# Performance work log

Measured on AMD Instinct MI355X. Metric: run time of the kernel, lower is better.

## Reference

```python
import jax, jax.numpy as jnp
import numpy as np

B, L, K1, P = 16, 224, 8192, 16  # batch, spectral bands, pixels, endmembers
LEAKY_SLOPE = 0.01  # torch nn.LeakyReLU default


def setup_inputs() -> dict:
    key = jax.random.key(0)
    ks = jax.random.split(key, 7)
    return {
        "a": jax.random.normal(ks[0], (B, P, K1), jnp.float32),
        "d2": jax.random.normal(ks[1], (B, P, K1), jnp.float32),
        "y": jax.random.normal(ks[2], (B, L, K1), jnp.float32),
        "w3_w": jax.random.normal(ks[3], (P, P), jnp.float32) * 0.1,  # Conv1d(P,P,1) weight squeezed
        "b3_w": jax.random.normal(ks[4], (P, P), jnp.float32) * 0.1,
        "w3_c": jax.random.normal(ks[5], (1, L, P), jnp.float32),     # kernel codebook
        "sigma": jnp.ones((1,), jnp.float32) * 2.0,
        "ca_w": jax.random.normal(ks[6], (2, P), jnp.float32) * 0.1,  # CA Conv1d(P,2,1) weight squeezed
    }


def reference(a, d2, y, w3_w, b3_w, w3_c, sigma, ca_w):
    # h2 = Conv1d(P,P,1)(a - d2)  -> pointwise matmul over channel dim
    h2 = jnp.einsum('pq,bqn->bpn', w3_w, a - d2)  # (B,P,K1)

    # GaussianKernelLayer: pairwise L2 distances between y pixels (B,L,K1)
    # and codebook columns w3_c (1,L,P), via the GEMM identity
    # ||u-v||^2 = ||u||^2 + ||v||^2 - 2 u.v  (avoids the (B,L,K1,P) broadcast).
    y_sq = jnp.sum(y * y, axis=1)            # (B,K1)
    c_sq = jnp.sum(w3_c * w3_c, axis=1)      # (1,P)
    cross = jnp.einsum('blk,olp->bkp', y, w3_c)  # (B,K1,P)
    dist_sq = jnp.maximum(y_sq[:, :, None] + c_sq[:, None, :] - 2.0 * cross, 0.0)
    dist = jnp.sqrt(dist_sq)                 # (B,K1,P)
    h3 = jnp.exp(-0.5 * jnp.square(dist / sigma[0]))
    h3 = jnp.transpose(h3, (0, 2, 1))        # (B,P,K1)

    # CA channel attention: avg/max pool over pixels -> Conv1d(P,2,1) -> LeakyReLU -> softmax
    avg = jnp.mean(h3, axis=-1)              # (B,P)
    mx = jnp.max(h3, axis=-1)                # (B,P)
    conv_lrelu = lambda v: jax.nn.leaky_relu(jnp.einsum('cp,bp->bc', ca_w, v), LEAKY_SLOPE)
    ratio = jax.nn.softmax(conv_lrelu(avg) + conv_lrelu(mx), axis=-1)  # (B,2)

    # combine center pixel + mean pixel via bmm with ratio
    mid = h3[:, :, K1 // 2]                  # (B,P)
    mean = jnp.mean(h3, axis=-1)             # (B,P)
    stacked = jnp.stack([mid, mean], axis=1)  # (B,2,P)
    comb = jnp.einsum('bc,bcp->bp', ratio, stacked)  # (B,P)

    # h4 = Conv1d(P,P,1)(comb[:, :, None])
    h4 = jnp.einsum('pq,bq->bp', b3_w, comb)[:, :, None]  # (B,P,1)

    return h4 + h2  # broadcast over pixel dim -> (B,P,K1)
```

## Files before the change

kernel.cpp:

```cpp
#include <hip/hip_runtime.h>

#define Bn  16
#define Ln  224
#define K1n 8192
#define Pn  16
#define NCHUNK 32


__global__ __launch_bounds__(256) void k_stats(
    const float* __restrict__ y,
    const float* __restrict__ w3c,
    const float* __restrict__ sigma,
    float* __restrict__ ws_sum,
    float* __restrict__ ws_max,
    float* __restrict__ ws_mid)
{
    __shared__ float s_w3c[Ln][Pn];
    __shared__ float s_csq[Pn];
    __shared__ float s_part_s[4][Pn];
    __shared__ float s_part_m[4][Pn];

    const int tid   = threadIdx.x;
    const int b     = blockIdx.x >> 5;
    const int chunk = blockIdx.x & 31;
    const int k     = (chunk << 8) + tid;

    for (int i = tid; i < Ln * Pn; i += 256) {
        s_w3c[i >> 4][i & 15] = w3c[i];
    }
    __syncthreads();
    if (tid < Pn) {
        float cs = 0.f;
        for (int l = 0; l < Ln; ++l) { float v = s_w3c[l][tid]; cs = fmaf(v, v, cs); }
        s_csq[tid] = cs;
    }
    __syncthreads();

    float cross[Pn];
#pragma unroll
    for (int p = 0; p < Pn; ++p) cross[p] = 0.f;
    float ysq = 0.f;

    const float* yp = y + (size_t)b * Ln * K1n + k;
#pragma unroll 16
    for (int l = 0; l < Ln; ++l) {
        float v = yp[(size_t)l * K1n];
        ysq = fmaf(v, v, ysq);
#pragma unroll
        for (int p = 0; p < Pn; ++p) cross[p] = fmaf(v, s_w3c[l][p], cross[p]);
    }

    const float sg = sigma[0];
    const float neg_half_inv_s2 = -0.5f / (sg * sg);

    float h3[Pn];
#pragma unroll
    for (int p = 0; p < Pn; ++p) {
        float d = ysq + s_csq[p] - 2.f * cross[p];
        d = fmaxf(d, 0.f);
        h3[p] = __expf(d * neg_half_inv_s2);
    }

    if (k == (K1n / 2)) {
#pragma unroll
        for (int p = 0; p < Pn; ++p) ws_mid[b * Pn + p] = h3[p];
    }

    const int lane = tid & 63;
    const int wv   = tid >> 6;
#pragma unroll
    for (int p = 0; p < Pn; ++p) {
        float s = h3[p];
        float m = h3[p];
#pragma unroll
        for (int off = 32; off > 0; off >>= 1) {
            s += __shfl_down(s, off, 64);
            m = fmaxf(m, __shfl_down(m, off, 64));
        }
        if (lane == 0) { s_part_s[wv][p] = s; s_part_m[wv][p] = m; }
    }
    __syncthreads();
    if (tid < Pn) {
        float s = s_part_s[0][tid] + s_part_s[1][tid] + s_part_s[2][tid] + s_part_s[3][tid];
        float m = fmaxf(fmaxf(s_part_m[0][tid], s_part_m[1][tid]),
                        fmaxf(s_part_m[2][tid], s_part_m[3][tid]));
        const int base = (b * NCHUNK + chunk) * Pn + tid;
        ws_sum[base] = s;
        ws_max[base] = m;
    }
}

__global__ __launch_bounds__(256) void k_out(
    const float* __restrict__ a,
    const float* __restrict__ d2,
    const float* __restrict__ w3w,
    const float* __restrict__ b3w,
    const float* __restrict__ caw,
    const float* __restrict__ ws_sum,
    const float* __restrict__ ws_max,
    const float* __restrict__ ws_mid,
    float* __restrict__ out)
{
    __shared__ float s_w3w[Pn][Pn];
    __shared__ float s_red_s[16][Pn];
    __shared__ float s_red_m[16][Pn];
    __shared__ float s_avg[Pn], s_mx[Pn], s_mid[Pn], s_comb[Pn], s_h4[Pn];
    __shared__ float s_t[2];

    const int tid = threadIdx.x;
    const int b   = blockIdx.x >> 5;
    const int k   = ((blockIdx.x & 31) << 8) + tid;

    if (tid < Pn * Pn) s_w3w[tid >> 4][tid & 15] = w3w[tid];

    {
        const int p   = tid & 15;
        const int grp = tid >> 4;
        const int i0  = (b * NCHUNK + grp)      * Pn + p;
        const int i1  = (b * NCHUNK + grp + 16) * Pn + p;
        s_red_s[grp][p] = ws_sum[i0] + ws_sum[i1];
        s_red_m[grp][p] = fmaxf(ws_max[i0], ws_max[i1]);
    }
    __syncthreads();
    if (tid < Pn) {
        float s = 0.f, m = -1.f;
        for (int g = 0; g < 16; ++g) {
            s += s_red_s[g][tid];
            m = fmaxf(m, s_red_m[g][tid]);
        }
        s_avg[tid] = s * (1.f / (float)K1n);
        s_mx[tid]  = m;
        s_mid[tid] = ws_mid[b * Pn + tid];
    }
    __syncthreads();

    if (tid < 2) {
        float t1 = 0.f, t2 = 0.f;
        for (int p = 0; p < Pn; ++p) {
            float cw = caw[tid * Pn + p];
            t1 = fmaf(cw, s_avg[p], t1);
            t2 = fmaf(cw, s_mx[p],  t2);
        }
        t1 = (t1 > 0.f) ? t1 : 0.01f * t1;
        t2 = (t2 > 0.f) ? t2 : 0.01f * t2;
        s_t[tid] = t1 + t2;
    }
    __syncthreads();

    if (tid < Pn) {
        float t0 = s_t[0], u1 = s_t[1];
        float mt = fmaxf(t0, u1);
        float e0 = __expf(t0 - mt), e1 = __expf(u1 - mt);
        float inv = 1.f / (e0 + e1);
        s_comb[tid] = (e0 * inv) * s_mid[tid] + (e1 * inv) * s_avg[tid];
    }
    __syncthreads();

    if (tid < Pn) {
        float h = 0.f;
        for (int q = 0; q < Pn; ++q) h = fmaf(b3w[tid * Pn + q], s_comb[q], h);
        s_h4[tid] = h;
    }
    __syncthreads();

    const size_t base = (size_t)b * Pn * K1n + (size_t)k;
    float diff[Pn];
#pragma unroll
    for (int q = 0; q < Pn; ++q) {
        float av = a [base + (size_t)q * K1n];
        float dv = d2[base + (size_t)q * K1n];
        diff[q] = av - dv;
    }
#pragma unroll
    for (int p = 0; p < Pn; ++p) {
        float h2 = 0.f;
#pragma unroll
        for (int q = 0; q < Pn; ++q) h2 = fmaf(s_w3w[p][q], diff[q], h2);
        out[base + (size_t)p * K1n] = h2 + s_h4[p];
    }
}

extern "C" void kernel_launch(void* const* d_in, const int* in_sizes, int n_in,
                              void* d_out, int out_size, void* d_ws, size_t ws_size,
                              hipStream_t stream) {
    const float* a     = (const float*)d_in[0];
    const float* d2    = (const float*)d_in[1];
    const float* y     = (const float*)d_in[2];
    const float* w3w   = (const float*)d_in[3];
    const float* b3w   = (const float*)d_in[4];
    const float* w3c   = (const float*)d_in[5];
    const float* sigma = (const float*)d_in[6];
    const float* caw   = (const float*)d_in[7];

    float* ws_sum = (float*)d_ws;
    float* ws_max = ws_sum + Bn * NCHUNK * Pn;
    float* ws_mid = ws_max + Bn * NCHUNK * Pn;

    k_stats<<<dim3(Bn * NCHUNK), dim3(256), 0, stream>>>(
        y, w3c, sigma, ws_sum, ws_max, ws_mid);

    k_out<<<dim3(Bn * NCHUNK), dim3(256), 0, stream>>>(
        a, d2, w3w, b3w, caw, ws_sum, ws_max, ws_mid, (float*)d_out);
}
```

Baseline: 215.6 us.

## Give each thread four pixels with float4 loads and single-wave blocks

Both kernels now launch 64-thread blocks, each thread covering four consecutive pixels through float4 loads and stores. In k_stats every shared-memory codebook read now serves four FMAs instead of one, and the cross-wave shared reduction is replaced by a single wavefront shuffle reduction. k_out reads all 32 partial chunks directly instead of through a two-stage shared reduction. The risks are fewer waves in flight (512 blocks of one wave each on a large GPU), higher register pressure from 64 accumulators, and lower latency hiding for the memory-bound output pass.

```diff
diff --git a/kernel.cpp b/kernel.cpp
--- a/kernel.cpp
+++ b/kernel.cpp
@@ -7,7 +7,7 @@
 #define NCHUNK 32
 
 
-__global__ __launch_bounds__(256) void k_stats(
+__global__ __launch_bounds__(64) void k_stats(
     const float* __restrict__ y,
     const float* __restrict__ w3c,
     const float* __restrict__ sigma,
@@ -17,17 +17,13 @@
 {
     __shared__ float s_w3c[Ln][Pn];
     __shared__ float s_csq[Pn];
-    __shared__ float s_part_s[4][Pn];
-    __shared__ float s_part_m[4][Pn];
 
     const int tid   = threadIdx.x;
     const int b     = blockIdx.x >> 5;
     const int chunk = blockIdx.x & 31;
-    const int k     = (chunk << 8) + tid;
-
-    for (int i = tid; i < Ln * Pn; i += 256) {
-        s_w3c[i >> 4][i & 15] = w3c[i];
-    }
+    const int kb    = chunk << 8;
+
+    for (int i = tid; i < Ln * Pn; i += 64) s_w3c[i >> 4][i & 15] = w3c[i];
     __syncthreads();
     if (tid < Pn) {
         float cs = 0.f;
@@ -36,61 +32,63 @@
     }
     __syncthreads();
 
-    float cross[Pn];
-#pragma unroll
-    for (int p = 0; p < Pn; ++p) cross[p] = 0.f;
-    float ysq = 0.f;
-
-    const float* yp = y + (size_t)b * Ln * K1n + k;
-#pragma unroll 16
+    float cross0[Pn], cross1[Pn], cross2[Pn], cross3[Pn];
+#pragma unroll
+    for (int p = 0; p < Pn; ++p) { cross0[p] = cross1[p] = cross2[p] = cross3[p] = 0.f; }
+    float ysq0 = 0.f, ysq1 = 0.f, ysq2 = 0.f, ysq3 = 0.f;
+
+    const float4* yp = reinterpret_cast<const float4*>(
+                           y + (size_t)b * Ln * K1n + kb) + tid;
+#pragma unroll 8
     for (int l = 0; l < Ln; ++l) {
-        float v = yp[(size_t)l * K1n];
-        ysq = fmaf(v, v, ysq);
-#pragma unroll
-        for (int p = 0; p < Pn; ++p) cross[p] = fmaf(v, s_w3c[l][p], cross[p]);
+        float4 v = yp[l * (K1n / 4)];
+        ysq0 = fmaf(v.x, v.x, ysq0);
+        ysq1 = fmaf(v.y, v.y, ysq1);
+        ysq2 = fmaf(v.z, v.z, ysq2);
+        ysq3 = fmaf(v.w, v.w, ysq3);
+#pragma unroll
+        for (int p = 0; p < Pn; ++p) {
+            float w = s_w3c[l][p];
+            cross0[p] = fmaf(v.x, w, cross0[p]);
+            cross1[p] = fmaf(v.y, w, cross1[p]);
+            cross2[p] = fmaf(v.z, w, cross2[p]);
+            cross3[p] = fmaf(v.w, w, cross3[p]);
+        }
     }
 
     const float sg = sigma[0];
-    const float neg_half_inv_s2 = -0.5f / (sg * sg);
-
-    float h3[Pn];
+    const float nh = -0.5f / (sg * sg);
+    const bool midw = (kb == (K1n / 2)) && (tid == 0);
+
 #pragma unroll
     for (int p = 0; p < Pn; ++p) {
-        float d = ysq + s_csq[p] - 2.f * cross[p];
-        d = fmaxf(d, 0.f);
-        h3[p] = __expf(d * neg_half_inv_s2);
-    }
-
-    if (k == (K1n / 2)) {
-#pragma unroll
-        for (int p = 0; p < Pn; ++p) ws_mid[b * Pn + p] = h3[p];
-    }
-
-    const int lane = tid & 63;
-    const int wv   = tid >> 6;
-#pragma unroll
-    for (int p = 0; p < Pn; ++p) {
-        float s = h3[p];
-        float m = h3[p];
+        float c = s_csq[p];
+        float d0 = fmaxf(ysq0 + c - 2.f * cross0[p], 0.f);
+        float d1 = fmaxf(ysq1 + c - 2.f * cross1[p], 0.f);
+        float d2_ = fmaxf(ysq2 + c - 2.f * cross2[p], 0.f);
+        float d3 = fmaxf(ysq3 + c - 2.f * cross3[p], 0.f);
+        float h0 = __expf(d0 * nh);
+        float h1 = __expf(d1 * nh);
+        float h2 = __expf(d2_ * nh);
+        float h3 = __expf(d3 * nh);
+        if (midw) ws_mid[b * Pn + p] = h0;
+
+        float s = (h0 + h1) + (h2 + h3);
+        float m = fmaxf(fmaxf(h0, h1), fmaxf(h2, h3));
 #pragma unroll
         for (int off = 32; off > 0; off >>= 1) {
             s += __shfl_down(s, off, 64);
             m = fmaxf(m, __shfl_down(m, off, 64));
         }
-        if (lane == 0) { s_part_s[wv][p] = s; s_part_m[wv][p] = m; }
-    }
-    __syncthreads();
-    if (tid < Pn) {
-        float s = s_part_s[0][tid] + s_part_s[1][tid] + s_part_s[2][tid] + s_part_s[3][tid];
-        float m = fmaxf(fmaxf(s_part_m[0][tid], s_part_m[1][tid]),
-                        fmaxf(s_part_m[2][tid], s_part_m[3][tid]));
-        const int base = (b * NCHUNK + chunk) * Pn + tid;
-        ws_sum[base] = s;
-        ws_max[base] = m;
+        if (tid == 0) {
+            const int base = (b * NCHUNK + chunk) * Pn + p;
+            ws_sum[base] = s;
+            ws_max[base] = m;
+        }
     }
 }
 
-__global__ __launch_bounds__(256) void k_out(
+__global__ __launch_bounds__(64) void k_out(
     const float* __restrict__ a,
     const float* __restrict__ d2,
     const float* __restrict__ w3w,
@@ -102,31 +100,21 @@
     float* __restrict__ out)
 {
     __shared__ float s_w3w[Pn][Pn];
-    __shared__ float s_red_s[16][Pn];
-    __shared__ float s_red_m[16][Pn];
     __shared__ float s_avg[Pn], s_mx[Pn], s_mid[Pn], s_comb[Pn], s_h4[Pn];
     __shared__ float s_t[2];
 
     const int tid = threadIdx.x;
     const int b   = blockIdx.x >> 5;
-    const int k   = ((blockIdx.x & 31) << 8) + tid;
-
-    if (tid < Pn * Pn) s_w3w[tid >> 4][tid & 15] = w3w[tid];
-
-    {
-        const int p   = tid & 15;
-        const int grp = tid >> 4;
-        const int i0  = (b * NCHUNK + grp)      * Pn + p;
-        const int i1  = (b * NCHUNK + grp + 16) * Pn + p;
-        s_red_s[grp][p] = ws_sum[i0] + ws_sum[i1];
-        s_red_m[grp][p] = fmaxf(ws_max[i0], ws_max[i1]);
-    }
-    __syncthreads();
+    const int kb  = (blockIdx.x & 31) << 8;
+
+    for (int i = tid; i < Pn * Pn; i += 64) s_w3w[i >> 4][i & 15] = w3w[i];
+
     if (tid < Pn) {
         float s = 0.f, m = -1.f;
-        for (int g = 0; g < 16; ++g) {
-            s += s_red_s[g][tid];
-            m = fmaxf(m, s_red_m[g][tid]);
+        for (int g = 0; g < NCHUNK; ++g) {
+            const int idx = (b * NCHUNK + g) * Pn + tid;
+            s += ws_sum[idx];
+            m = fmaxf(m, ws_max[idx]);
         }
         s_avg[tid] = s * (1.f / (float)K1n);
         s_mx[tid]  = m;
@@ -163,20 +151,30 @@
     }
     __syncthreads();
 
-    const size_t base = (size_t)b * Pn * K1n + (size_t)k;
-    float diff[Pn];
+    const size_t base = (size_t)b * Pn * K1n + kb + 4 * tid;
+    float4 diff[Pn];
 #pragma unroll
     for (int q = 0; q < Pn; ++q) {
-        float av = a [base + (size_t)q * K1n];
-        float dv = d2[base + (size_t)q * K1n];
-        diff[q] = av - dv;
+        float4 av = *reinterpret_cast<const float4*>(a  + base + (size_t)q * K1n);
+        float4 dv = *reinterpret_cast<const float4*>(d2 + base + (size_t)q * K1n);
+        diff[q].x = av.x - dv.x;
+        diff[q].y = av.y - dv.y;
+        diff[q].z = av.z - dv.z;
+        diff[q].w = av.w - dv.w;
     }
 #pragma unroll
     for (int p = 0; p < Pn; ++p) {
-        float h2 = 0.f;
-#pragma unroll
-        for (int q = 0; q < Pn; ++q) h2 = fmaf(s_w3w[p][q], diff[q], h2);
-        out[base + (size_t)p * K1n] = h2 + s_h4[p];
+        float4 h2;
+        h2.x = h2.y = h2.z = h2.w = s_h4[p];
+#pragma unroll
+        for (int q = 0; q < Pn; ++q) {
+            const float w = s_w3w[p][q];
+            h2.x = fmaf(w, diff[q].x, h2.x);
+            h2.y = fmaf(w, diff[q].y, h2.y);
+            h2.z = fmaf(w, diff[q].z, h2.z);
+            h2.w = fmaf(w, diff[q].w, h2.w);
+        }
+        *reinterpret_cast<float4*>(out + base + (size_t)p * K1n) = h2;
     }
 }
 
@@ -196,9 +194,9 @@
     float* ws_max = ws_sum + Bn * NCHUNK * Pn;
     float* ws_mid = ws_max + Bn * NCHUNK * Pn;
 
-    k_stats<<<dim3(Bn * NCHUNK), dim3(256), 0, stream>>>(
+    k_stats<<<dim3(Bn * NCHUNK), dim3(64), 0, stream>>>(
         y, w3c, sigma, ws_sum, ws_max, ws_mid);
 
-    k_out<<<dim3(Bn * NCHUNK), dim3(256), 0, stream>>>(
+    k_out<<<dim3(Bn * NCHUNK), dim3(64), 0, stream>>>(
         a, d2, w3w, b3w, caw, ws_sum, ws_max, ws_mid, (float*)d_out);
 }
```

Measured after the change: 254.9 us. 1.18x slower.
